# Kernel optimization log

Hardware: AMD Instinct MI355X
Metric: run time of the kernel (lower is better)

Reference implementation:

```python
import jax, jax.numpy as jnp
import numpy as np

N_NODES = 100000
N_EDGES = 1600000
IN_CH = 128
HID = 128
OUT_CH = 10
NUM_LAYERS = 3
NUM_GRAPHS = 512


def _glorot(key, shape):
    fan_in, fan_out = shape[0], shape[1]
    lim = jnp.sqrt(6.0 / (fan_in + fan_out))
    return jax.random.uniform(key, shape, jnp.float32, -lim, lim)


def setup_inputs() -> dict:
    key = jax.random.key(0)
    ks = jax.random.split(key, 20)
    inp = {}
    inp["x"] = jax.random.normal(ks[0], (N_NODES, IN_CH), jnp.float32)
    inp["edge_index"] = jax.random.randint(ks[1], (2, N_EDGES), 0, N_NODES, jnp.int64)
    inp["batch"] = jnp.sort(jax.random.randint(ks[2], (N_NODES,), 0, NUM_GRAPHS, jnp.int64))
    # GIN layer MLP params: Linear(in, hid) -> ReLU -> Linear(hid, hid)
    kidx = 3
    for l in range(NUM_LAYERS):
        d_in = IN_CH if l == 0 else HID
        inp[f"w1_{l}"] = _glorot(ks[kidx], (d_in, HID)); kidx += 1
        inp[f"b1_{l}"] = jnp.zeros((HID,), jnp.float32)
        inp[f"w2_{l}"] = _glorot(ks[kidx], (HID, HID)); kidx += 1
        inp[f"b2_{l}"] = jnp.zeros((HID,), jnp.float32)
    inp["lin_w"] = _glorot(ks[kidx], (HID, OUT_CH))
    inp["lin_b"] = jnp.zeros((OUT_CH,), jnp.float32)
    return inp


def _gin_forward(x, src, dst, batch, layer_params, lin_w, lin_b):
    h = x
    n_layers = len(layer_params)
    for i, (w1, b1, w2, b2) in enumerate(layer_params):
        # GINConv: (1 + eps) * h + sum_{j in N(i)} h_j, eps = 0
        agg = jax.ops.segment_sum(h[src], dst, num_segments=N_NODES)
        z = h + agg
        # MLP: Linear -> ReLU -> Linear
        h = jnp.maximum(z @ w1 + b1, 0.0) @ w2 + b2
        if i < n_layers - 1:  # inter-layer ReLU (PyG BasicGNN act)
            h = jnp.maximum(h, 0.0)
    # global_add_pool over batch ids -> [NUM_GRAPHS, HID]
    pooled = jax.ops.segment_sum(h, batch, num_segments=NUM_GRAPHS)
    # dropout(p=0.5) is identity in eval mode
    return pooled @ lin_w + lin_b


def reference(x, edge_index, batch,
              w1_0, b1_0, w2_0, b2_0,
              w1_1, b1_1, w2_1, b2_1,
              w1_2, b1_2, w2_2, b2_2,
              lin_w, lin_b):
    src, dst = edge_index[0], edge_index[1]
    layer_params = [(w1_0, b1_0, w2_0, b2_0),
                    (w1_1, b1_1, w2_1, b2_1),
                    (w1_2, b1_2, w2_2, b2_2)]
    return _gin_forward(x, src, dst, batch, layer_params, lin_w, lin_b)
```

## Files before the change

### kernel.cpp

```cpp
#include <hip/hip_runtime.h>

#define CH 128
#define OUTC 10
#define NB 256
#define BCAP 10240
#define PCHUNK 2048
#define PQ2 132
#define FBM 64

typedef __attribute__((ext_vector_type(8))) short short8;
typedef __attribute__((ext_vector_type(4))) short short4v;
typedef __attribute__((ext_vector_type(16))) float f32x16;


__device__ inline unsigned short f2bf(float f) {
    unsigned u = __builtin_bit_cast(unsigned, f);
    u += 0x7fffu + ((u >> 16) & 1u);
    return (unsigned short)(u >> 16);
}
__device__ inline float bflo(unsigned u) { return __builtin_bit_cast(float, u << 16); }
__device__ inline float bfhi(unsigned u) { return __builtin_bit_cast(float, u & 0xffff0000u); }

__device__ inline void acc8(float* a, const uint4& v) {
    a[0] += bflo(v.x); a[1] += bfhi(v.x);
    a[2] += bflo(v.y); a[3] += bfhi(v.y);
    a[4] += bflo(v.z); a[5] += bfhi(v.z);
    a[6] += bflo(v.w); a[7] += bfhi(v.w);
}


struct WPtrs { const float* s[6]; unsigned short* d[6]; };

__global__ void prep_part_kernel(const int* __restrict__ src, const int* __restrict__ dst,
                                 int* __restrict__ bucketCnt, unsigned* __restrict__ pairs, int E,
                                 int nPartBlk,
                                 const float4* __restrict__ x4, uint2* __restrict__ xb, int n4,
                                 int nConvBlk, WPtrs p,
                                 uint4* __restrict__ pooled4, int nPooled4) {
    __shared__ int hist[NB];
    __shared__ int base[NB];
    __shared__ int cur[NB];
    int tid = threadIdx.x;
    int b = blockIdx.x;

    if (b < nPartBlk) {
        int e0 = b * PCHUNK;
        hist[tid] = 0;
        __syncthreads();
        #pragma unroll
        for (int i = 0; i < PCHUNK / 256; ++i) {
            int e = e0 + tid + i * 256;
            if (e < E) atomicAdd(&hist[dst[e] >> 9], 1);
        }
        __syncthreads();
        {
            int c = hist[tid];
            base[tid] = (c > 0) ? atomicAdd(&bucketCnt[tid], c) : 0;
            cur[tid] = 0;
        }
        __syncthreads();
        #pragma unroll
        for (int i = 0; i < PCHUNK / 256; ++i) {
            int e = e0 + tid + i * 256;
            if (e < E) {
                int d = dst[e];
                int bkt = d >> 9;
                int pos = base[bkt] + atomicAdd(&cur[bkt], 1);
                if (pos < BCAP)
                    pairs[bkt * BCAP + pos] = ((unsigned)(d & 511) << 17) | (unsigned)src[e];
            }
        }
    } else if (b < nPartBlk + nConvBlk) {
        int i = (b - nPartBlk) * 256 + tid;
        if (i < n4) {
            float4 v = x4[i];
            uint2 o;
            o.x = (unsigned)f2bf(v.x) | ((unsigned)f2bf(v.y) << 16);
            o.y = (unsigned)f2bf(v.z) | ((unsigned)f2bf(v.w) << 16);
            xb[i] = o;
        }
    } else if (b < nPartBlk + nConvBlk + 384) {
        int bb = b - nPartBlk - nConvBlk;
        int m = bb >> 6;
        int i = (bb & 63) * 256 + tid;
        int j = i & 7;
        int l = (i >> 3) & 63;
        int k0 = (i >> 9) & 7;
        int ct = (i >> 12) & 3;
        int k = k0 * 16 + ((l >> 5) << 3) + j;
        int nn = ct * 32 + (l & 31);
        p.d[m][i] = f2bf(p.s[m][k * CH + nn]);
    } else {
        int i = (b - nPartBlk - nConvBlk - 384) * 256 + tid;
        if (i < nPooled4) pooled4[i] = make_uint4(0, 0, 0, 0);
    }
}


__launch_bounds__(256)
__global__ void build_csr_kernel(const unsigned* __restrict__ pairs, const int* __restrict__ bucketCnt,
                                 int* __restrict__ offs, int* __restrict__ csr, int N) {
    __shared__ int bsm[NB];
    __shared__ int ldeg[512];
    __shared__ int s0[512], s1[512];
    __shared__ int lexc[512];
    __shared__ int lcur[512];
    __shared__ int lcsr[BCAP];

    int b = blockIdx.x;
    int node0 = b << 9;
    if (node0 >= N) return;
    int nLocal = min(512, N - node0);
    int tid = threadIdx.x;

    bsm[tid] = bucketCnt[tid];
    __syncthreads();
    for (int off = 1; off < NB; off <<= 1) {
        int t = (tid >= off) ? bsm[tid - off] : 0;
        __syncthreads();
        bsm[tid] += t;
        __syncthreads();
    }
    int cnt = min(bucketCnt[b], BCAP);
    int gbase = bsm[b] - bucketCnt[b];

    for (int i = tid; i < 512; i += 256) ldeg[i] = 0;
    __syncthreads();
    for (int i = tid; i < cnt; i += 256)
        atomicAdd(&ldeg[pairs[b * BCAP + i] >> 17], 1);
    __syncthreads();

    for (int i = tid; i < 512; i += 256) s0[i] = ldeg[i];
    __syncthreads();
    int* sp = s0; int* dp = s1;
    for (int off = 1; off < 512; off <<= 1) {
        for (int i = tid; i < 512; i += 256)
            dp[i] = sp[i] + ((i >= off) ? sp[i - off] : 0);
        __syncthreads();
        int* t = sp; sp = dp; dp = t;
    }
    for (int i = tid; i < 512; i += 256) {
        int ex = sp[i] - ldeg[i];
        lexc[i] = ex;
        lcur[i] = ex;
    }
    __syncthreads();

    for (int i = tid; i < cnt; i += 256) {
        unsigned w = pairs[b * BCAP + i];
        int ppos = atomicAdd(&lcur[w >> 17], 1);
        lcsr[ppos] = (int)(w & 0x1ffffu);
    }
    __syncthreads();

    for (int i = tid; i < cnt; i += 256) csr[gbase + i] = lcsr[i];
    for (int i = tid; i < nLocal; i += 256) offs[node0 + i] = gbase + lexc[i];
    if (tid == 0 && node0 + nLocal == N) offs[N] = gbase + cnt;
}


template <int L, int RELU, int POOL>
__launch_bounds__(512)
__global__ void fused_gin_kernel(const uint4* __restrict__ h4,
                                 const int* __restrict__ offs, const int* __restrict__ csr,
                                 const unsigned short* __restrict__ w1s, const float* __restrict__ b1,
                                 const unsigned short* __restrict__ w2s, const float* __restrict__ b2,
                                 unsigned short* __restrict__ hout,
                                 const int* __restrict__ batch, float* __restrict__ pooled,
                                 int n) {
    __shared__ __align__(16) unsigned short zs[FBM * PQ2];

    int tid = threadIdx.x;
    int row0 = blockIdx.x * FBM;

    {
        int gl = tid & 15;
        int grp = tid >> 4;
        #pragma unroll
        for (int it = 0; it < 2; ++it) {
            int rr = grp + 32 * it;
            int node = row0 + rr;
            unsigned o0 = 0, o1 = 0, o2 = 0, o3 = 0;
            if (node < n) {
                int beg = offs[node], end = offs[node + 1];
                float a[8];
                uint4 self = h4[node * 16 + gl];
                a[0] = bflo(self.x); a[1] = bfhi(self.x);
                a[2] = bflo(self.y); a[3] = bfhi(self.y);
                a[4] = bflo(self.z); a[5] = bfhi(self.z);
                a[6] = bflo(self.w); a[7] = bfhi(self.w);
                int e = beg;
                for (; e + 4 <= end; e += 4) {
                    int s0 = csr[e], s1 = csr[e + 1], s2 = csr[e + 2], s3 = csr[e + 3];
                    uint4 v0 = h4[s0 * 16 + gl];
                    uint4 v1 = h4[s1 * 16 + gl];
                    uint4 v2 = h4[s2 * 16 + gl];
                    uint4 v3 = h4[s3 * 16 + gl];
                    acc8(a, v0); acc8(a, v1); acc8(a, v2); acc8(a, v3);
                }
                for (; e < end; ++e) {
                    uint4 v = h4[csr[e] * 16 + gl];
                    acc8(a, v);
                }
                o0 = (unsigned)f2bf(a[0]) | ((unsigned)f2bf(a[1]) << 16);
                o1 = (unsigned)f2bf(a[2]) | ((unsigned)f2bf(a[3]) << 16);
                o2 = (unsigned)f2bf(a[4]) | ((unsigned)f2bf(a[5]) << 16);
                o3 = (unsigned)f2bf(a[6]) | ((unsigned)f2bf(a[7]) << 16);
            }
            *(uint2*)&zs[rr * PQ2 + gl * 8]     = make_uint2(o0, o1);
            *(uint2*)&zs[rr * PQ2 + gl * 8 + 4] = make_uint2(o2, o3);
        }
    }
    __syncthreads();

    int wv = tid >> 6;
    int lane = tid & 63;
    int l31 = lane & 31;
    int kh = lane >> 5;
    int rt = wv & 1;
    int ct = wv >> 1;
    int arow = rt * 32 + l31;

    f32x16 acc;
    {
        float bv = b1[ct * 32 + l31];
        #pragma unroll
        for (int r = 0; r < 16; ++r) acc[r] = bv;
    }
    #pragma unroll
    for (int k0 = 0; k0 < 8; ++k0) {
        short8 afr;
        {
            short4v lo = *(const short4v*)&zs[arow * PQ2 + k0 * 16 + kh * 8];
            short4v hi = *(const short4v*)&zs[arow * PQ2 + k0 * 16 + kh * 8 + 4];
            afr = (short8){lo[0], lo[1], lo[2], lo[3], hi[0], hi[1], hi[2], hi[3]};
        }
        short8 bfr = *(const short8*)&w1s[(((ct * 8 + k0) * 64) + lane) * 8];
        acc = __builtin_amdgcn_mfma_f32_32x32x16_bf16(afr, bfr, acc, 0, 0, 0);
    }
    __syncthreads();

    #pragma unroll
    for (int reg = 0; reg < 16; ++reg) {
        int crow = (reg & 3) + 8 * (reg >> 2) + 4 * kh;
        zs[(rt * 32 + crow) * PQ2 + ct * 32 + l31] = f2bf(fmaxf(acc[reg], 0.f));
    }
    __syncthreads();

    {
        float bv = b2[ct * 32 + l31];
        #pragma unroll
        for (int r = 0; r < 16; ++r) acc[r] = bv;
    }
    #pragma unroll
    for (int k0 = 0; k0 < 8; ++k0) {
        short8 afr;
        {
            short4v lo = *(const short4v*)&zs[arow * PQ2 + k0 * 16 + kh * 8];
            short4v hi = *(const short4v*)&zs[arow * PQ2 + k0 * 16 + kh * 8 + 4];
            afr = (short8){lo[0], lo[1], lo[2], lo[3], hi[0], hi[1], hi[2], hi[3]};
        }
        short8 bfr = *(const short8*)&w2s[(((ct * 8 + k0) * 64) + lane) * 8];
        acc = __builtin_amdgcn_mfma_f32_32x32x16_bf16(afr, bfr, acc, 0, 0, 0);
    }
    __syncthreads();

    #pragma unroll
    for (int reg = 0; reg < 16; ++reg) {
        int crow = (reg & 3) + 8 * (reg >> 2) + 4 * kh;
        float v = acc[reg];
        if (RELU) v = fmaxf(v, 0.f);
        zs[(rt * 32 + crow) * PQ2 + ct * 32 + l31] = f2bf(v);
    }
    __syncthreads();

    if (!POOL) {
        for (int i = tid; i < FBM * 16; i += 512) {
            int r = i >> 4, c = i & 15;
            int row = row0 + r;
            if (row < n) {
                uint2 a = *(const uint2*)&zs[r * PQ2 + c * 8];
                uint2 b = *(const uint2*)&zs[r * PQ2 + c * 8 + 4];
                ((uint4*)hout)[row * 16 + c] = make_uint4(a.x, a.y, b.x, b.y);
            }
        }
    } else {
        int c2 = tid & 63;
        int rs = tid >> 6;
        float a0 = 0.f, a1 = 0.f;
        int prevg = -1;
        #pragma unroll
        for (int i = 0; i < FBM / 8; ++i) {
            int r = rs + 8 * i;
            int row = row0 + r;
            if (row >= n) break;
            int g = batch[row];
            if (g != prevg) {
                if (prevg >= 0) {
                    atomicAdd(&pooled[prevg * CH + 2 * c2], a0);
                    atomicAdd(&pooled[prevg * CH + 2 * c2 + 1], a1);
                }
                prevg = g; a0 = 0.f; a1 = 0.f;
            }
            unsigned v = *(const unsigned*)&zs[r * PQ2 + c2 * 2];
            a0 += bflo(v); a1 += bfhi(v);
        }
        if (prevg >= 0) {
            atomicAdd(&pooled[prevg * CH + 2 * c2], a0);
            atomicAdd(&pooled[prevg * CH + 2 * c2 + 1], a1);
        }
    }
}


__global__ void final_linear_kernel(const float* __restrict__ pooled, const float* __restrict__ lin_w,
                                    const float* __restrict__ lin_b, float* __restrict__ out) {
    int g = blockIdx.x;
    int tid = threadIdx.x;
    __shared__ float pl[CH];
    pl[tid] = pooled[g * CH + tid];
    __syncthreads();
    if (tid < OUTC) {
        float a = lin_b[tid];
        #pragma unroll 16
        for (int c = 0; c < CH; ++c) a = fmaf(pl[c], lin_w[c * OUTC + tid], a);
        out[g * OUTC + tid] = a;
    }
}


static inline size_t aln(size_t x) { return (x + 255) & ~size_t(255); }

extern "C" void kernel_launch(void* const* d_in, const int* in_sizes, int n_in,
                              void* d_out, int out_size, void* d_ws, size_t ws_size,
                              hipStream_t stream) {
    const float* x      = (const float*)d_in[0];
    const int*   ei     = (const int*)d_in[1];
    const int*   batch  = (const int*)d_in[2];
    const float* w1[3]  = {(const float*)d_in[3], (const float*)d_in[7],  (const float*)d_in[11]};
    const float* b1[3]  = {(const float*)d_in[4], (const float*)d_in[8],  (const float*)d_in[12]};
    const float* w2[3]  = {(const float*)d_in[5], (const float*)d_in[9],  (const float*)d_in[13]};
    const float* b2[3]  = {(const float*)d_in[6], (const float*)d_in[10], (const float*)d_in[14]};
    const float* lin_w  = (const float*)d_in[15];
    const float* lin_b  = (const float*)d_in[16];
    float* out = (float*)d_out;

    int E = in_sizes[1] / 2;
    int N = in_sizes[2];
    int n_graphs = out_size / OUTC;
    const int* src = ei;
    const int* dst = ei + E;

    char* p = (char*)d_ws;
    int* bucketCnt  = (int*)p; p += aln(NB * 4);
    unsigned* pairs = (unsigned*)p; p += aln((size_t)NB * BCAP * 4);
    int* offs       = (int*)p; p += aln((size_t)(N + 1) * 4);
    int* csr        = (int*)p; p += aln((size_t)E * 4);
    unsigned short* xb = (unsigned short*)p; p += aln((size_t)N * CH * 2);
    unsigned short* hA = (unsigned short*)p; p += aln((size_t)N * CH * 2);
    unsigned short* hB = (unsigned short*)p; p += aln((size_t)N * CH * 2);
    float* pooled = (float*)p; p += aln((size_t)n_graphs * CH * 4);
    unsigned short* wt[6];
    for (int i = 0; i < 6; ++i) { wt[i] = (unsigned short*)p; p += aln((size_t)CH * CH * 2); }
    (void)ws_size; (void)n_in;

    hipMemsetAsync(bucketCnt, 0, NB * 4, stream);

    int n4 = N * CH / 4;
    int nConvBlk = (n4 + 255) / 256;
    int nPartBlk = (E + PCHUNK - 1) / PCHUNK;
    int nPooled4 = n_graphs * CH / 4;
    int nZeroBlk = (nPooled4 + 255) / 256;
    WPtrs wp;
    for (int l = 0; l < 3; ++l) {
        wp.s[2 * l] = w1[l];     wp.d[2 * l] = wt[2 * l];
        wp.s[2 * l + 1] = w2[l]; wp.d[2 * l + 1] = wt[2 * l + 1];
    }
    prep_part_kernel<<<nPartBlk + nConvBlk + 384 + nZeroBlk, 256, 0, stream>>>(
        src, dst, bucketCnt, pairs, E, nPartBlk,
        (const float4*)x, (uint2*)xb, n4, nConvBlk, wp,
        (uint4*)pooled, nPooled4);

    build_csr_kernel<<<NB, 256, 0, stream>>>(pairs, bucketCnt, offs, csr, N);

    int fblk = (N + FBM - 1) / FBM;

    fused_gin_kernel<0, 1, 0><<<fblk, 512, 0, stream>>>((const uint4*)xb, offs, csr,
        wt[0], b1[0], wt[1], b2[0], hA, batch, pooled, N);
    fused_gin_kernel<1, 1, 0><<<fblk, 512, 0, stream>>>((const uint4*)hA, offs, csr,
        wt[2], b1[1], wt[3], b2[1], hB, batch, pooled, N);
    fused_gin_kernel<2, 0, 1><<<fblk, 512, 0, stream>>>((const uint4*)hB, offs, csr,
        wt[4], b1[2], wt[5], b2[2], (unsigned short*)nullptr, batch, pooled, N);

    final_linear_kernel<<<n_graphs, CH, 0, stream>>>(pooled, lin_w, lin_b, out);
}
```

Before: 384.7 us.

## Balance edge aggregation across thread groups with edge-range splitting and LDS atomics

Replaces the one-node-per-group neighbour aggregation with an edge-balanced split. Each of 32 thread groups takes an equal slice of the block's CSR edge range, binary-searches its starting node, and flushes partial sums into an fp32 LDS tile with shared-memory atomics at node boundaries. The tile is seeded with self features first, and bf16 conversion moves to the MFMA A-fragment load. This targets load imbalance from uneven degrees, at the cost of LDS atomics, a larger fp32 tile, and conversion work inside the GEMM loop.

```diff
diff --git a/kernel.cpp b/kernel.cpp
--- a/kernel.cpp
+++ b/kernel.cpp
@@ -5,6 +5,7 @@
 #define NB 256
 #define BCAP 10240
 #define PCHUNK 2048
+#define PQF 130
 #define PQ2 132
 #define FBM 64
 
@@ -168,47 +169,83 @@
                                  unsigned short* __restrict__ hout,
                                  const int* __restrict__ batch, float* __restrict__ pooled,
                                  int n) {
-    __shared__ __align__(16) unsigned short zs[FBM * PQ2];
+    __shared__ __align__(16) float zf[FBM * PQF];
+    __shared__ int offsL[FBM + 1];
+
+    unsigned short* zs = (unsigned short*)zf;
 
     int tid = threadIdx.x;
     int row0 = blockIdx.x * FBM;
+    int gl = tid & 15;
+    int grp = tid >> 4;
+
+    for (int i = tid; i <= FBM; i += 512) offsL[i] = offs[min(row0 + i, n)];
+    #pragma unroll
+    for (int it = 0; it < 2; ++it) {
+        int rr = grp + 32 * it;
+        int node = row0 + rr;
+        float v0 = 0.f, v1 = 0.f, v2 = 0.f, v3 = 0.f, v4 = 0.f, v5 = 0.f, v6 = 0.f, v7 = 0.f;
+        if (node < n) {
+            uint4 s = h4[node * 16 + gl];
+            v0 = bflo(s.x); v1 = bfhi(s.x);
+            v2 = bflo(s.y); v3 = bfhi(s.y);
+            v4 = bflo(s.z); v5 = bfhi(s.z);
+            v6 = bflo(s.w); v7 = bfhi(s.w);
+        }
+        float* zr = &zf[rr * PQF + gl * 8];
+        *(float2*)&zr[0] = make_float2(v0, v1);
+        *(float2*)&zr[2] = make_float2(v2, v3);
+        *(float2*)&zr[4] = make_float2(v4, v5);
+        *(float2*)&zr[6] = make_float2(v6, v7);
+    }
+    __syncthreads();
 
     {
-        int gl = tid & 15;
-        int grp = tid >> 4;
-        #pragma unroll
-        for (int it = 0; it < 2; ++it) {
-            int rr = grp + 32 * it;
-            int node = row0 + rr;
-            unsigned o0 = 0, o1 = 0, o2 = 0, o3 = 0;
-            if (node < n) {
-                int beg = offs[node], end = offs[node + 1];
-                float a[8];
-                uint4 self = h4[node * 16 + gl];
-                a[0] = bflo(self.x); a[1] = bfhi(self.x);
-                a[2] = bflo(self.y); a[3] = bfhi(self.y);
-                a[4] = bflo(self.z); a[5] = bfhi(self.z);
-                a[6] = bflo(self.w); a[7] = bfhi(self.w);
-                int e = beg;
-                for (; e + 4 <= end; e += 4) {
-                    int s0 = csr[e], s1 = csr[e + 1], s2 = csr[e + 2], s3 = csr[e + 3];
-                    uint4 v0 = h4[s0 * 16 + gl];
-                    uint4 v1 = h4[s1 * 16 + gl];
-                    uint4 v2 = h4[s2 * 16 + gl];
-                    uint4 v3 = h4[s3 * 16 + gl];
-                    acc8(a, v0); acc8(a, v1); acc8(a, v2); acc8(a, v3);
+        int eBeg = offsL[0];
+        int eEnd = offsL[FBM];
+        int total = eEnd - eBeg;
+        int chunk = (total + 31) >> 5;
+        int gs = eBeg + grp * chunk;
+        int ge = min(gs + chunk, eEnd);
+        if (gs < ge) {
+            int lo = 0, hi = FBM - 1;
+            while (lo < hi) { int mid = (lo + hi + 1) >> 1; if (offsL[mid] <= gs) lo = mid; else hi = mid - 1; }
+            int nd = lo;
+            int ndEnd = offsL[nd + 1];
+            float a[8] = {0.f, 0.f, 0.f, 0.f, 0.f, 0.f, 0.f, 0.f};
+            int e = gs;
+            for (; e + 4 <= ge; e += 4) {
+                int s0 = csr[e], s1 = csr[e + 1], s2 = csr[e + 2], s3 = csr[e + 3];
+                uint4 w0 = h4[s0 * 16 + gl];
+                uint4 w1 = h4[s1 * 16 + gl];
+                uint4 w2 = h4[s2 * 16 + gl];
+                uint4 w3 = h4[s3 * 16 + gl];
+                #pragma unroll
+                for (int i = 0; i < 4; ++i) {
+                    if (e + i >= ndEnd) {
+                        float* zr = &zf[nd * PQF + gl * 8];
+                        #pragma unroll
+                        for (int j = 0; j < 8; ++j) { atomicAdd(&zr[j], a[j]); a[j] = 0.f; }
+                        do { ++nd; ndEnd = offsL[nd + 1]; } while (e + i >= ndEnd);
+                    }
+                    acc8(a, i == 0 ? w0 : (i == 1 ? w1 : (i == 2 ? w2 : w3)));
                 }
-                for (; e < end; ++e) {
-                    uint4 v = h4[csr[e] * 16 + gl];
-                    acc8(a, v);
+            }
+            for (; e < ge; ++e) {
+                if (e >= ndEnd) {
+                    float* zr = &zf[nd * PQF + gl * 8];
+                    #pragma unroll
+                    for (int j = 0; j < 8; ++j) { atomicAdd(&zr[j], a[j]); a[j] = 0.f; }
+                    do { ++nd; ndEnd = offsL[nd + 1]; } while (e >= ndEnd);
                 }
-                o0 = (unsigned)f2bf(a[0]) | ((unsigned)f2bf(a[1]) << 16);
-                o1 = (unsigned)f2bf(a[2]) | ((unsigned)f2bf(a[3]) << 16);
-                o2 = (unsigned)f2bf(a[4]) | ((unsigned)f2bf(a[5]) << 16);
-                o3 = (unsigned)f2bf(a[6]) | ((unsigned)f2bf(a[7]) << 16);
-            }
-            *(uint2*)&zs[rr * PQ2 + gl * 8]     = make_uint2(o0, o1);
-            *(uint2*)&zs[rr * PQ2 + gl * 8 + 4] = make_uint2(o2, o3);
+                uint4 w = h4[csr[e] * 16 + gl];
+                acc8(a, w);
+            }
+            {
+                float* zr = &zf[nd * PQF + gl * 8];
+                #pragma unroll
+                for (int j = 0; j < 8; ++j) atomicAdd(&zr[j], a[j]);
+            }
         }
     }
     __syncthreads();
@@ -231,9 +268,13 @@
     for (int k0 = 0; k0 < 8; ++k0) {
         short8 afr;
         {
-            short4v lo = *(const short4v*)&zs[arow * PQ2 + k0 * 16 + kh * 8];
-            short4v hi = *(const short4v*)&zs[arow * PQ2 + k0 * 16 + kh * 8 + 4];
-            afr = (short8){lo[0], lo[1], lo[2], lo[3], hi[0], hi[1], hi[2], hi[3]};
+            const float* zr = &zf[arow * PQF + k0 * 16 + kh * 8];
+            float2 f0 = *(const float2*)&zr[0];
+            float2 f1 = *(const float2*)&zr[2];
+            float2 f2 = *(const float2*)&zr[4];
+            float2 f3 = *(const float2*)&zr[6];
+            afr = (short8){(short)f2bf(f0.x), (short)f2bf(f0.y), (short)f2bf(f1.x), (short)f2bf(f1.y),
+                           (short)f2bf(f2.x), (short)f2bf(f2.y), (short)f2bf(f3.x), (short)f2bf(f3.y)};
         }
         short8 bfr = *(const short8*)&w1s[(((ct * 8 + k0) * 64) + lane) * 8];
         acc = __builtin_amdgcn_mfma_f32_32x32x16_bf16(afr, bfr, acc, 0, 0, 0);
```

Result: slower. 562.4 us (+46.2%).

## Use 256-thread GIN kernel for middle layer and enlarge partition chunk

Applied to the files above, without the earlier changes.

Adds a 256-thread variant of the fused GIN layer kernel in which each wave computes two 32-column MFMA tiles and each thread gathers four rows instead of two. It is used only for the middle layer, with the aggregation loop factored into a shared helper. The partition chunk grows from 2048 to 8192 edges per block, and the partition loops are no longer force-unrolled, so fewer blocks each do more work. This trades per-block thread parallelism during the memory-bound gather for more independent work per thread and fewer blocks. It risks lower latency hiding in the gather and less parallelism in partitioning.

```diff
diff --git a/kernel.cpp b/kernel.cpp
--- a/kernel.cpp
+++ b/kernel.cpp
@@ -4,7 +4,7 @@
 #define OUTC 10
 #define NB 256
 #define BCAP 10240
-#define PCHUNK 2048
+#define PCHUNK 8192
 #define PQ2 132
 #define FBM 64
 
@@ -26,6 +26,35 @@
     a[2] += bflo(v.y); a[3] += bfhi(v.y);
     a[4] += bflo(v.z); a[5] += bfhi(v.z);
     a[6] += bflo(v.w); a[7] += bfhi(v.w);
+}
+
+__device__ inline void gather_row(const uint4* __restrict__ h4, const int* __restrict__ offs,
+                                  const int* __restrict__ csr, int node, int gl,
+                                  unsigned& o0, unsigned& o1, unsigned& o2, unsigned& o3) {
+    int beg = offs[node], end = offs[node + 1];
+    float a[8];
+    uint4 self = h4[node * 16 + gl];
+    a[0] = bflo(self.x); a[1] = bfhi(self.x);
+    a[2] = bflo(self.y); a[3] = bfhi(self.y);
+    a[4] = bflo(self.z); a[5] = bfhi(self.z);
+    a[6] = bflo(self.w); a[7] = bfhi(self.w);
+    int e = beg;
+    for (; e + 4 <= end; e += 4) {
+        int s0 = csr[e], s1 = csr[e + 1], s2 = csr[e + 2], s3 = csr[e + 3];
+        uint4 v0 = h4[s0 * 16 + gl];
+        uint4 v1 = h4[s1 * 16 + gl];
+        uint4 v2 = h4[s2 * 16 + gl];
+        uint4 v3 = h4[s3 * 16 + gl];
+        acc8(a, v0); acc8(a, v1); acc8(a, v2); acc8(a, v3);
+    }
+    for (; e < end; ++e) {
+        uint4 v = h4[csr[e] * 16 + gl];
+        acc8(a, v);
+    }
+    o0 = (unsigned)f2bf(a[0]) | ((unsigned)f2bf(a[1]) << 16);
+    o1 = (unsigned)f2bf(a[2]) | ((unsigned)f2bf(a[3]) << 16);
+    o2 = (unsigned)f2bf(a[4]) | ((unsigned)f2bf(a[5]) << 16);
+    o3 = (unsigned)f2bf(a[6]) | ((unsigned)f2bf(a[7]) << 16);
 }
 
 
@@ -47,7 +76,6 @@
         int e0 = b * PCHUNK;
         hist[tid] = 0;
         __syncthreads();
-        #pragma unroll
         for (int i = 0; i < PCHUNK / 256; ++i) {
             int e = e0 + tid + i * 256;
             if (e < E) atomicAdd(&hist[dst[e] >> 9], 1);
@@ -59,7 +87,6 @@
             cur[tid] = 0;
         }
         __syncthreads();
-        #pragma unroll
         for (int i = 0; i < PCHUNK / 256; ++i) {
             int e = e0 + tid + i * 256;
             if (e < E) {
@@ -181,32 +208,7 @@
             int rr = grp + 32 * it;
             int node = row0 + rr;
             unsigned o0 = 0, o1 = 0, o2 = 0, o3 = 0;
-            if (node < n) {
-                int beg = offs[node], end = offs[node + 1];
-                float a[8];
-                uint4 self = h4[node * 16 + gl];
-                a[0] = bflo(self.x); a[1] = bfhi(self.x);
-                a[2] = bflo(self.y); a[3] = bfhi(self.y);
-                a[4] = bflo(self.z); a[5] = bfhi(self.z);
-                a[6] = bflo(self.w); a[7] = bfhi(self.w);
-                int e = beg;
-                for (; e + 4 <= end; e += 4) {
-                    int s0 = csr[e], s1 = csr[e + 1], s2 = csr[e + 2], s3 = csr[e + 3];
-                    uint4 v0 = h4[s0 * 16 + gl];
-                    uint4 v1 = h4[s1 * 16 + gl];
-                    uint4 v2 = h4[s2 * 16 + gl];
-                    uint4 v3 = h4[s3 * 16 + gl];
-                    acc8(a, v0); acc8(a, v1); acc8(a, v2); acc8(a, v3);
-                }
-                for (; e < end; ++e) {
-                    uint4 v = h4[csr[e] * 16 + gl];
-                    acc8(a, v);
-                }
-                o0 = (unsigned)f2bf(a[0]) | ((unsigned)f2bf(a[1]) << 16);
-                o1 = (unsigned)f2bf(a[2]) | ((unsigned)f2bf(a[3]) << 16);
-                o2 = (unsigned)f2bf(a[4]) | ((unsigned)f2bf(a[5]) << 16);
-                o3 = (unsigned)f2bf(a[6]) | ((unsigned)f2bf(a[7]) << 16);
-            }
+            if (node < n) gather_row(h4, offs, csr, node, gl, o0, o1, o2, o3);
             *(uint2*)&zs[rr * PQ2 + gl * 8]     = make_uint2(o0, o1);
             *(uint2*)&zs[rr * PQ2 + gl * 8 + 4] = make_uint2(o2, o3);
         }
@@ -313,6 +315,114 @@
 }
 
 
+template <int L, int RELU>
+__launch_bounds__(256)
+__global__ void fused_gin256_kernel(const uint4* __restrict__ h4,
+                                    const int* __restrict__ offs, const int* __restrict__ csr,
+                                    const unsigned short* __restrict__ w1s, const float* __restrict__ b1,
+                                    const unsigned short* __restrict__ w2s, const float* __restrict__ b2,
+                                    unsigned short* __restrict__ hout, int n) {
+    __shared__ __align__(16) unsigned short zs[FBM * PQ2];
+
+    int tid = threadIdx.x;
+    int row0 = blockIdx.x * FBM;
+
+    {
+        int gl = tid & 15;
+        int grp = tid >> 4;
+        #pragma unroll
+        for (int it = 0; it < 4; ++it) {
+            int rr = grp + 16 * it;
+            int node = row0 + rr;
+            unsigned o0 = 0, o1 = 0, o2 = 0, o3 = 0;
+            if (node < n) gather_row(h4, offs, csr, node, gl, o0, o1, o2, o3);
+            *(uint2*)&zs[rr * PQ2 + gl * 8]     = make_uint2(o0, o1);
+            *(uint2*)&zs[rr * PQ2 + gl * 8 + 4] = make_uint2(o2, o3);
+        }
+    }
+    __syncthreads();
+
+    int wv = tid >> 6;
+    int lane = tid & 63;
+    int l31 = lane & 31;
+    int kh = lane >> 5;
+    int rt = wv & 1;
+    int ct0 = (wv >> 1) * 2;
+    int arow = rt * 32 + l31;
+
+    f32x16 acc0, acc1;
+    {
+        float bv0 = b1[ct0 * 32 + l31];
+        float bv1 = b1[(ct0 + 1) * 32 + l31];
+        #pragma unroll
+        for (int r = 0; r < 16; ++r) { acc0[r] = bv0; acc1[r] = bv1; }
+    }
+    #pragma unroll
+    for (int k0 = 0; k0 < 8; ++k0) {
+        short8 afr;
+        {
+            short4v lo = *(const short4v*)&zs[arow * PQ2 + k0 * 16 + kh * 8];
+            short4v hi = *(const short4v*)&zs[arow * PQ2 + k0 * 16 + kh * 8 + 4];
+            afr = (short8){lo[0], lo[1], lo[2], lo[3], hi[0], hi[1], hi[2], hi[3]};
+        }
+        short8 bf0 = *(const short8*)&w1s[(((ct0 * 8 + k0) * 64) + lane) * 8];
+        short8 bf1 = *(const short8*)&w1s[((((ct0 + 1) * 8 + k0) * 64) + lane) * 8];
+        acc0 = __builtin_amdgcn_mfma_f32_32x32x16_bf16(afr, bf0, acc0, 0, 0, 0);
+        acc1 = __builtin_amdgcn_mfma_f32_32x32x16_bf16(afr, bf1, acc1, 0, 0, 0);
+    }
+    __syncthreads();
+
+    #pragma unroll
+    for (int reg = 0; reg < 16; ++reg) {
+        int crow = (reg & 3) + 8 * (reg >> 2) + 4 * kh;
+        zs[(rt * 32 + crow) * PQ2 + ct0 * 32 + l31]       = f2bf(fmaxf(acc0[reg], 0.f));
+        zs[(rt * 32 + crow) * PQ2 + (ct0 + 1) * 32 + l31] = f2bf(fmaxf(acc1[reg], 0.f));
+    }
+    __syncthreads();
+
+    {
+        float bv0 = b2[ct0 * 32 + l31];
+        float bv1 = b2[(ct0 + 1) * 32 + l31];
+        #pragma unroll
+        for (int r = 0; r < 16; ++r) { acc0[r] = bv0; acc1[r] = bv1; }
+    }
+    #pragma unroll
+    for (int k0 = 0; k0 < 8; ++k0) {
+        short8 afr;
+        {
+            short4v lo = *(const short4v*)&zs[arow * PQ2 + k0 * 16 + kh * 8];
+            short4v hi = *(const short4v*)&zs[arow * PQ2 + k0 * 16 + kh * 8 + 4];
+            afr = (short8){lo[0], lo[1], lo[2], lo[3], hi[0], hi[1], hi[2], hi[3]};
+        }
+        short8 bf0 = *(const short8*)&w2s[(((ct0 * 8 + k0) * 64) + lane) * 8];
+        short8 bf1 = *(const short8*)&w2s[((((ct0 + 1) * 8 + k0) * 64) + lane) * 8];
+        acc0 = __builtin_amdgcn_mfma_f32_32x32x16_bf16(afr, bf0, acc0, 0, 0, 0);
+        acc1 = __builtin_amdgcn_mfma_f32_32x32x16_bf16(afr, bf1, acc1, 0, 0, 0);
+    }
+    __syncthreads();
+
+    #pragma unroll
+    for (int reg = 0; reg < 16; ++reg) {
+        int crow = (reg & 3) + 8 * (reg >> 2) + 4 * kh;
+        float v0 = acc0[reg], v1 = acc1[reg];
+        if (RELU) { v0 = fmaxf(v0, 0.f); v1 = fmaxf(v1, 0.f); }
+        zs[(rt * 32 + crow) * PQ2 + ct0 * 32 + l31]       = f2bf(v0);
+        zs[(rt * 32 + crow) * PQ2 + (ct0 + 1) * 32 + l31] = f2bf(v1);
+    }
+    __syncthreads();
+
+    for (int i = tid; i < FBM * 16; i += 256) {
+        int r = i >> 4, c = i & 15;
+        int row = row0 + r;
+        if (row < n) {
+            uint2 a = *(const uint2*)&zs[r * PQ2 + c * 8];
+            uint2 b = *(const uint2*)&zs[r * PQ2 + c * 8 + 4];
+            ((uint4*)hout)[row * 16 + c] = make_uint4(a.x, a.y, b.x, b.y);
+        }
+    }
+}
+
+
 __global__ void final_linear_kernel(const float* __restrict__ pooled, const float* __restrict__ lin_w,
                                     const float* __restrict__ lin_b, float* __restrict__ out) {
     int g = blockIdx.x;
@@ -387,8 +497,8 @@
 
     fused_gin_kernel<0, 1, 0><<<fblk, 512, 0, stream>>>((const uint4*)xb, offs, csr,
         wt[0], b1[0], wt[1], b2[0], hA, batch, pooled, N);
-    fused_gin_kernel<1, 1, 0><<<fblk, 512, 0, stream>>>((const uint4*)hA, offs, csr,
-        wt[2], b1[1], wt[3], b2[1], hB, batch, pooled, N);
+    fused_gin256_kernel<1, 1><<<fblk, 256, 0, stream>>>((const uint4*)hA, offs, csr,
+        wt[2], b1[1], wt[3], b2[1], hB, N);
     fused_gin_kernel<2, 0, 1><<<fblk, 512, 0, stream>>>((const uint4*)hB, offs, csr,
         wt[4], b1[2], wt[5], b2[2], (unsigned short*)nullptr, batch, pooled, N);
 
```

New measurement: 392.4 us. 2.0% more time.
